# Optimization experiments

Measured on AMD Instinct MI355X. Metric: run time of the kernel, lower is better.

## Reference

```python
import jax, jax.numpy as jnp
import numpy as np

L, V, P, D, H, F = 6, 50257, 1024, 1024, 16, 4096
DH = D // H
EPS = 1e-5


def setup_inputs() -> dict:
    key = jax.random.key(0)
    ks = jax.random.split(key, 8)
    s = 0.02  # init scale to keep activations sane across layers
    inp = {
        "input_ids": jax.random.randint(ks[0], (2, 1024), 0, V),
        "wte": jax.random.normal(ks[1], (V, D), jnp.float32) * s,
        "wpe": jax.random.normal(ks[2], (P, D), jnp.float32) * s,
        "ln1_g": jnp.ones((L, D), jnp.float32),
        "ln1_b": jnp.zeros((L, D), jnp.float32),
        "wq": jax.random.normal(ks[3], (L, D, D), jnp.float32) * s,
        "bq": jnp.zeros((L, D), jnp.float32),
        "wk": jax.random.normal(ks[4], (L, D, D), jnp.float32) * s,
        "bk": jnp.zeros((L, D), jnp.float32),
        "wv": jax.random.normal(ks[5], (L, D, D), jnp.float32) * s,
        "bv": jnp.zeros((L, D), jnp.float32),
        "wo": jax.random.normal(jax.random.fold_in(key, 10), (L, D, D), jnp.float32) * s,
        "bo": jnp.zeros((L, D), jnp.float32),
        "ln2_g": jnp.ones((L, D), jnp.float32),
        "ln2_b": jnp.zeros((L, D), jnp.float32),
        "w1": jax.random.normal(ks[6], (L, D, F), jnp.float32) * s,
        "b1": jnp.zeros((L, F), jnp.float32),
        "w2": jax.random.normal(ks[7], (L, F, D), jnp.float32) * s,
        "b2": jnp.zeros((L, D), jnp.float32),
        "lnf_g": jnp.ones((D,), jnp.float32),
        "lnf_b": jnp.zeros((D,), jnp.float32),
    }
    return inp


def _ln(x, g, b):
    m = jnp.mean(x, axis=-1, keepdims=True)
    v = jnp.mean(jnp.square(x - m), axis=-1, keepdims=True)
    return (x - m) * jax.lax.rsqrt(v + EPS) * g + b


def _block(x, p):
    (g1, be1, wq, bq, wk, bk, wv, bv, wo, bo, g2, be2, w1, b1, w2, b2) = p
    B, T, _ = x.shape
    h = _ln(x, g1, be1)
    q = (h @ wq + bq).reshape(B, T, H, DH)
    k = (h @ wk + bk).reshape(B, T, H, DH)
    v = (h @ wv + bv).reshape(B, T, H, DH)
    scores = jnp.einsum("bqhd,bkhd->bhqk", q, k) * (1.0 / np.sqrt(DH))
    attn = jax.nn.softmax(scores, axis=-1)  # NOTE: no causal mask (as in source)
    o = jnp.einsum("bhqk,bkhd->bqhd", attn, v).reshape(B, T, D)
    x = x + o @ wo + bo
    h2 = _ln(x, g2, be2)
    x = x + jax.nn.gelu(h2 @ w1 + b1, approximate=False) @ w2 + b2
    return x


def reference(input_ids, wte, wpe, ln1_g, ln1_b, wq, bq, wk, bk, wv, bv,
              wo, bo, ln2_g, ln2_b, w1, b1, w2, b2, lnf_g, lnf_b):
    T = input_ids.shape[1]
    x = wte[input_ids] + wpe[:T]  # [B,T,D]
    params = (ln1_g, ln1_b, wq, bq, wk, bk, wv, bv, wo, bo,
              ln2_g, ln2_b, w1, b1, w2, b2)

    def step(x, p):
        return _block(x, p), None

    x, _ = jax.lax.scan(step, x, params)
    return _ln(x, lnf_g, lnf_b)
```

## Files before the change

kernel.cpp:

```cpp
#include <hip/hip_runtime.h>
#include <hip/hip_bf16.h>
#include <math.h>

#define DV 1024
#define FF 4096
#define NLAY 6
#define NH 16
#define TT 1024
#define NTOK 2048

typedef float f32x4 __attribute__((ext_vector_type(4)));
typedef short bf16x8 __attribute__((ext_vector_type(8)));
typedef unsigned short u16;
typedef u16 u16x4 __attribute__((ext_vector_type(4)));
typedef u16 u16x8 __attribute__((ext_vector_type(8)));

__device__ __forceinline__ u16 f2b(float f) {
  unsigned u = __float_as_uint(f);
  unsigned r = (u + 0x7fffu + ((u >> 16) & 1u)) >> 16;
  return (u16)r;
}
__device__ __forceinline__ float b2f(u16 u) {
  return __uint_as_float(((unsigned)u) << 16);
}

__device__ __forceinline__ void gload_lds16(const void* g, void* lds) {
  __builtin_amdgcn_global_load_lds(
      (const __attribute__((address_space(1))) void*)g,
      (__attribute__((address_space(3))) void*)lds, 16, 0, 0);
}

__global__ __launch_bounds__(256) void embed_ln_k(const int* __restrict__ ids,
                                                  const float* __restrict__ wte,
                                                  const float* __restrict__ wpe,
                                                  const float* __restrict__ gg,
                                                  const float* __restrict__ bb,
                                                  float* __restrict__ X,
                                                  u16* __restrict__ outb) {
  int row = blockIdx.x, tid = threadIdx.x;
  int t = row & (TT - 1);
  int id = ids[row];
  f32x4 a = *(const f32x4*)(wte + (size_t)id * DV + tid * 4);
  f32x4 p = *(const f32x4*)(wpe + (size_t)t * DV + tid * 4);
  f32x4 v = a + p;
  *(f32x4*)(X + (size_t)row * DV + tid * 4) = v;
  float s1 = v[0] + v[1] + v[2] + v[3];
  float s2 = v[0] * v[0] + v[1] * v[1] + v[2] * v[2] + v[3] * v[3];
#pragma unroll
  for (int o = 32; o >= 1; o >>= 1) {
    s1 += __shfl_xor(s1, o);
    s2 += __shfl_xor(s2, o);
  }
  __shared__ float sh[8];
  int w = tid >> 6;
  if ((tid & 63) == 0) { sh[w] = s1; sh[w + 4] = s2; }
  __syncthreads();
  s1 = sh[0] + sh[1] + sh[2] + sh[3];
  s2 = sh[4] + sh[5] + sh[6] + sh[7];
  float mean = s1 * (1.0f / DV);
  float var = s2 * (1.0f / DV) - mean * mean;
  float rstd = rsqrtf(var + 1e-5f);
  f32x4 gv = *(const f32x4*)(gg + tid * 4);
  f32x4 bv = *(const f32x4*)(bb + tid * 4);
  u16x4 r;
#pragma unroll
  for (int i = 0; i < 4; ++i) r[i] = f2b((v[i] - mean) * rstd * gv[i] + bv[i]);
  *(u16x4*)(outb + (size_t)row * DV + tid * 4) = r;
}

template <int OUTF>
__global__ __launch_bounds__(256) void ln_k(const float* __restrict__ X,
                                            const float* __restrict__ gg,
                                            const float* __restrict__ bb,
                                            u16* __restrict__ outb,
                                            float* __restrict__ outf) {
  int row = blockIdx.x, tid = threadIdx.x;
  f32x4 v = *(const f32x4*)(X + (size_t)row * DV + tid * 4);
  float s1 = v[0] + v[1] + v[2] + v[3];
  float s2 = v[0] * v[0] + v[1] * v[1] + v[2] * v[2] + v[3] * v[3];
#pragma unroll
  for (int o = 32; o >= 1; o >>= 1) {
    s1 += __shfl_xor(s1, o);
    s2 += __shfl_xor(s2, o);
  }
  __shared__ float sh[8];
  int w = tid >> 6;
  if ((tid & 63) == 0) { sh[w] = s1; sh[w + 4] = s2; }
  __syncthreads();
  s1 = sh[0] + sh[1] + sh[2] + sh[3];
  s2 = sh[4] + sh[5] + sh[6] + sh[7];
  float mean = s1 * (1.0f / DV);
  float var = s2 * (1.0f / DV) - mean * mean;
  float rstd = rsqrtf(var + 1e-5f);
  f32x4 gv = *(const f32x4*)(gg + tid * 4);
  f32x4 bv = *(const f32x4*)(bb + tid * 4);
  f32x4 o;
#pragma unroll
  for (int i = 0; i < 4; ++i) o[i] = (v[i] - mean) * rstd * gv[i] + bv[i];
  if (OUTF) {
    *(f32x4*)(outf + (size_t)row * DV + tid * 4) = o;
  } else {
    u16x4 r = {f2b(o[0]), f2b(o[1]), f2b(o[2]), f2b(o[3])};
    *(u16x4*)(outb + (size_t)row * DV + tid * 4) = r;
  }
}

template <int NS, int OUTF>
__global__ __launch_bounds__(256) void reduce_ln_k(
    float* __restrict__ X, const u16* __restrict__ pp,
    const float* __restrict__ bias, const float* __restrict__ gg,
    const float* __restrict__ bb, u16* __restrict__ outb,
    float* __restrict__ outf) {
  int row = blockIdx.x, tid = threadIdx.x;
  size_t off = (size_t)row * DV + tid * 4;
  f32x4 v = *(const f32x4*)(X + off);
  if (NS > 0) {
    f32x4 bvv = *(const f32x4*)(bias + tid * 4);
    v += bvv;
#pragma unroll
    for (int s = 0; s < NS; ++s) {
      u16x4 pv = *(const u16x4*)(pp + (size_t)s * NTOK * DV + off);
      v[0] += b2f(pv[0]); v[1] += b2f(pv[1]);
      v[2] += b2f(pv[2]); v[3] += b2f(pv[3]);
    }
    *(f32x4*)(X + off) = v;
  }
  float s1 = v[0] + v[1] + v[2] + v[3];
  float s2 = v[0] * v[0] + v[1] * v[1] + v[2] * v[2] + v[3] * v[3];
#pragma unroll
  for (int o = 32; o >= 1; o >>= 1) {
    s1 += __shfl_xor(s1, o);
    s2 += __shfl_xor(s2, o);
  }
  __shared__ float sh[8];
  int w = tid >> 6;
  if ((tid & 63) == 0) { sh[w] = s1; sh[w + 4] = s2; }
  __syncthreads();
  s1 = sh[0] + sh[1] + sh[2] + sh[3];
  s2 = sh[4] + sh[5] + sh[6] + sh[7];
  float mean = s1 * (1.0f / DV);
  float var = s2 * (1.0f / DV) - mean * mean;
  float rstd = rsqrtf(var + 1e-5f);
  f32x4 gv = *(const f32x4*)(gg + tid * 4);
  f32x4 bv = *(const f32x4*)(bb + tid * 4);
  f32x4 o;
#pragma unroll
  for (int i = 0; i < 4; ++i) o[i] = (v[i] - mean) * rstd * gv[i] + bv[i];
  if (OUTF) {
    *(f32x4*)(outf + off) = o;
  } else {
    u16x4 r = {f2b(o[0]), f2b(o[1]), f2b(o[2]), f2b(o[3])};
    *(u16x4*)(outb + off) = r;
  }
}

__global__ __launch_bounds__(256) void transw_k(const float* __restrict__ wq,
                                                const float* __restrict__ wk,
                                                const float* __restrict__ wv,
                                                const float* __restrict__ wo,
                                                const float* __restrict__ w1,
                                                const float* __restrict__ w2,
                                                u16* __restrict__ WT) {
  int lay = blockIdx.y;
  size_t oDD = (size_t)lay * DV * DV, oDF = (size_t)lay * DV * FF;
  u16* WTL = WT + (size_t)lay * 12 * 1024 * 1024;
  int bid = blockIdx.x;
  const float* src;
  u16* dst;
  int K, N, tile;
  if (bid < 256) {
    int which = bid >> 6;
    src = (which == 0 ? wq : which == 1 ? wk : which == 2 ? wv : wo) + oDD;
    dst = WTL + (size_t)which * (DV * DV);
    K = DV; N = DV; tile = bid & 63;
  } else if (bid < 512) {
    src = w1 + oDF; dst = WTL + (size_t)4 * (DV * DV); K = DV; N = FF; tile = bid - 256;
  } else {
    src = w2 + oDF; dst = WTL + (size_t)8 * (DV * DV); K = FF; N = DV; tile = bid - 512;
  }
  int ntc = N >> 8;
  int tr = tile / ntc, tc = tile - tr * ntc;
  int k0 = tr * 64, n0 = tc * 256;
  __shared__ u16 ts[64][258];
  int tid = threadIdx.x, l = tid & 63, w = tid >> 6;
  f32x4 vv[16];
#pragma unroll
  for (int i = 0; i < 16; ++i)
    vv[i] = *(const f32x4*)(src + (size_t)(k0 + i * 4 + w) * N + n0 + l * 4);
#pragma unroll
  for (int i = 0; i < 16; ++i) {
    u16x4 c = {f2b(vv[i][0]), f2b(vv[i][1]), f2b(vv[i][2]), f2b(vv[i][3])};
    *(u16x4*)(&ts[i * 4 + w][l * 4]) = c;
  }
  __syncthreads();
  int kk = (tid & 7) * 8, nn = tid >> 3;
#pragma unroll
  for (int j = 0; j < 8; ++j) {
    int n = j * 32 + nn;
    u16x8 ov;
#pragma unroll
    for (int m = 0; m < 8; ++m) ov[m] = ts[kk + m][n];
    *(u16x8*)(dst + (size_t)(n0 + n) * K + k0 + kk) = ov;
  }
}

template <int EPI>
__global__ __launch_bounds__(256) void gemm_k(
    const u16* __restrict__ A, const u16* __restrict__ Wt,
    const float* __restrict__ b0, const float* __restrict__ b1,
    const float* __restrict__ b2v, u16* __restrict__ o0, u16* __restrict__ o1,
    u16* __restrict__ o2t, u16* __restrict__ op, float* __restrict__ of,
    const float* __restrict__ res, int M, int N, int K, int KS) {
  int z = blockIdx.z;
  const u16* W = Wt;
  const float* bias = b0;
  u16* outb = o0;
  if (EPI == 0) {
    W = Wt + (size_t)z * N * K;
    bias = z == 0 ? b0 : z == 1 ? b1 : b2v;
    outb = z == 0 ? o0 : o1;
  }
  int gx = gridDim.x, nwg = gx * gridDim.y;
  int lin = blockIdx.y * gx + blockIdx.x;
  int cpx = nwg >> 3;
  int swz = (lin & 7) * cpx + (lin >> 3);
  int bm = (swz % gx) * 128, bn = (swz / gx) * 128;
  int kbeg = (EPI == 3) ? z * KS : 0;
  int klen = (EPI == 3) ? KS : K;
  __shared__ __attribute__((aligned(16))) u16 SM[32768];
  u16* As = SM;
  u16* Bs = SM + 16384;
  u16* Cs = SM;
  int tid = threadIdx.x, l = tid & 63, w = tid >> 6;
  int q = l & 15, g = l >> 4;
  int wm = (w >> 1) * 64, wn = (w & 1) * 64;
  int srow = w * 32 + (l >> 3);
  int scol = (((l & 7) ^ ((l >> 3) & 7))) * 8;
  const u16* Ab = A + (size_t)(bm + srow) * K + kbeg + scol;
  const u16* Wb = W + (size_t)(bn + srow) * K + kbeg + scol;
  f32x4 acc[4][4] = {};
  int nk = klen >> 6;
#pragma unroll
  for (int i = 0; i < 4; ++i) {
    gload_lds16(Ab + (size_t)i * 8 * K, &As[(w * 32 + i * 8) * 64]);
    gload_lds16(Wb + (size_t)i * 8 * K, &Bs[(w * 32 + i * 8) * 64]);
  }
  __syncthreads();
  for (int t = 0; t < nk; ++t) {
    int cur = t & 1;
    if (t + 1 < nk) {
      int ko = (t + 1) * 64;
#pragma unroll
      for (int i = 0; i < 4; ++i) {
        gload_lds16(Ab + (size_t)i * 8 * K + ko,
                    &As[(cur ^ 1) * 8192 + (w * 32 + i * 8) * 64]);
        gload_lds16(Wb + (size_t)i * 8 * K + ko,
                    &Bs[(cur ^ 1) * 8192 + (w * 32 + i * 8) * 64]);
      }
    }
#pragma unroll
    for (int kk = 0; kk < 2; ++kk) {
      bf16x8 af[4], bfr[4];
#pragma unroll
      for (int f = 0; f < 4; ++f) {
        int ra = wm + f * 16 + q, rb = wn + f * 16 + q;
        af[f]  = *(const bf16x8*)(&As[cur * 8192 + ra * 64 + ((kk * 4 + g) ^ (ra & 7)) * 8]);
        bfr[f] = *(const bf16x8*)(&Bs[cur * 8192 + rb * 64 + ((kk * 4 + g) ^ (rb & 7)) * 8]);
      }
#pragma unroll
      for (int fm = 0; fm < 4; ++fm)
#pragma unroll
        for (int fn = 0; fn < 4; ++fn)
          acc[fm][fn] = __builtin_amdgcn_mfma_f32_16x16x32_bf16(af[fm], bfr[fn],
                                                                acc[fm][fn], 0, 0, 0);
    }
    __syncthreads();
  }
  if (EPI == 2) {
#pragma unroll
    for (int fm = 0; fm < 4; ++fm)
#pragma unroll
      for (int fn = 0; fn < 4; ++fn) {
        int gcol = bn + wn + fn * 16 + q;
        int growb = bm + wm + fm * 16 + g * 4;
        float bv = bias[gcol];
#pragma unroll
        for (int r = 0; r < 4; ++r)
          of[(size_t)(growb + r) * N + gcol] = res[(size_t)(growb + r) * N + gcol]
                                               + acc[fm][fn][r] + bv;
      }
    return;
  }
  bool tr = (EPI == 0 && z == 2);
#pragma unroll
  for (int fm = 0; fm < 4; ++fm) {
#pragma unroll
    for (int fn = 0; fn < 4; ++fn) {
      int cL = wn + fn * 16 + q;
      float bv = (EPI == 3) ? 0.0f : bias[bn + cL];
#pragma unroll
      for (int r = 0; r < 4; ++r) {
        int rL = wm + fm * 16 + g * 4 + r;
        float v = acc[fm][fn][r] + bv;
        if (EPI == 1) v = 0.5f * v * (1.0f + erff(v * 0.70710678118f));
        if (tr) Cs[cL * 132 + rL] = f2b(v);
        else    Cs[rL * 132 + cL] = f2b(v);
      }
    }
  }
  __syncthreads();
  {
    int rowL = tid >> 4, c8 = (tid & 15) * 8;
#pragma unroll
    for (int p = 0; p < 8; ++p) {
      int row = p * 16 + rowL;
      u16x4 lo = *(const u16x4*)(&Cs[row * 132 + c8]);
      u16x4 hi = *(const u16x4*)(&Cs[row * 132 + c8 + 4]);
      u16x8 ov = {lo[0], lo[1], lo[2], lo[3], hi[0], hi[1], hi[2], hi[3]};
      if (tr) {
        *(u16x8*)(o2t + (size_t)(bn + row) * M + bm + c8) = ov;
      } else if (EPI == 3) {
        *(u16x8*)(op + (size_t)z * M * N + (size_t)(bm + row) * N + bn + c8) = ov;
      } else {
        *(u16x8*)(outb + (size_t)(bm + row) * N + bn + c8) = ov;
      }
    }
  }
}

__global__ __launch_bounds__(256) void attn_k(const u16* __restrict__ Q,
                                              const u16* __restrict__ Kb,
                                              const u16* __restrict__ Vt,
                                              u16* __restrict__ O) {
  int bid = blockIdx.x;
  int qt = bid & 15, h = (bid >> 4) & 15, b = bid >> 8;
  int tid = threadIdx.x, l = tid & 63, w = tid >> 6;
  int q = l & 15, g = l >> 4;
  int tokbase = b * TT;
  int qbase = tokbase + qt * 64 + w * 16;
  __shared__ __attribute__((aligned(16))) u16 Ks[2][32 * 64];
  __shared__ __attribute__((aligned(16))) u16 Vs[2][64 * 32];
  __shared__ __attribute__((aligned(16))) u16 Ps[4][512];
  bf16x8 qf[2];
  {
    int qrow = qbase + q;
#pragma unroll
    for (int half = 0; half < 2; ++half)
      qf[half] = *(const bf16x8*)(Q + (size_t)qrow * DV + h * 64 + half * 32 + g * 8);
  }
  int key_s = w * 8 + (l >> 3), c_s = l & 7;
  const u16* ksrc = Kb + (size_t)(tokbase + key_s) * DV + h * 64 + ((c_s ^ (key_s & 7)) * 8);
  int dl = w * 16 + (l >> 2), c2 = l & 3;
  const u16* vsrc = Vt + (size_t)(h * 64 + dl) * NTOK + tokbase + ((c2 ^ (dl & 3)) * 8);
  f32x4 oacc[4] = {};
  float m_run = -INFINITY, l_run = 0.0f;
  gload_lds16(ksrc, &Ks[0][w * 512]);
  gload_lds16(vsrc, &Vs[0][w * 512]);
  __syncthreads();
  for (int kbk = 0; kbk < TT / 32; ++kbk) {
    int cur = kbk & 1;
    if (kbk + 1 < TT / 32) {
      gload_lds16(ksrc + (size_t)(kbk + 1) * 32 * DV, &Ks[cur ^ 1][w * 512]);
      gload_lds16(vsrc + (kbk + 1) * 32, &Vs[cur ^ 1][w * 512]);
    }
    f32x4 s[2] = {};
#pragma unroll
    for (int kt = 0; kt < 2; ++kt)
#pragma unroll
      for (int half = 0; half < 2; ++half) {
        int row = kt * 16 + q;
        int chunk = (half * 4 + g) ^ (row & 7);
        bf16x8 kf = *(const bf16x8*)(&Ks[cur][row * 64 + chunk * 8]);
        s[kt] = __builtin_amdgcn_mfma_f32_16x16x32_bf16(kf, qf[half], s[kt], 0, 0, 0);
      }
    float tmax = -INFINITY;
#pragma unroll
    for (int kt = 0; kt < 2; ++kt)
#pragma unroll
      for (int r = 0; r < 4; ++r) {
        s[kt][r] *= 0.125f;
        tmax = fmaxf(tmax, s[kt][r]);
      }
    tmax = fmaxf(tmax, __shfl_xor(tmax, 16));
    tmax = fmaxf(tmax, __shfl_xor(tmax, 32));
    float m_new = fmaxf(m_run, tmax);
    float corr = __expf(m_run - m_new);
    float psum = 0.0f;
    u16 pb[2][4];
#pragma unroll
    for (int kt = 0; kt < 2; ++kt)
#pragma unroll
      for (int r = 0; r < 4; ++r) {
        float p = __expf(s[kt][r] - m_new);
        psum += p;
        pb[kt][r] = f2b(p);
      }
    psum += __shfl_xor(psum, 16);
    psum += __shfl_xor(psum, 32);
    l_run = l_run * corr + psum;
    m_run = m_new;
#pragma unroll
    for (int kt = 0; kt < 2; ++kt) {
      u16x4 pv4 = {pb[kt][0], pb[kt][1], pb[kt][2], pb[kt][3]};
      *(u16x4*)(&Ps[w][q * 32 + ((kt * 4 + g) ^ (q & 7)) * 4]) = pv4;
    }
    float corr4[4];
#pragma unroll
    for (int r = 0; r < 4; ++r) corr4[r] = __shfl(corr, g * 4 + r);
#pragma unroll
    for (int nt = 0; nt < 4; ++nt)
#pragma unroll
      for (int r = 0; r < 4; ++r) oacc[nt][r] *= corr4[r];
    u16x4 a0 = *(const u16x4*)(&Ps[w][q * 32 + ((2 * g) ^ (q & 7)) * 4]);
    u16x4 a1 = *(const u16x4*)(&Ps[w][q * 32 + ((2 * g + 1) ^ (q & 7)) * 4]);
    bf16x8 pa = {(short)a0[0], (short)a0[1], (short)a0[2], (short)a0[3],
                 (short)a1[0], (short)a1[1], (short)a1[2], (short)a1[3]};
#pragma unroll
    for (int nt = 0; nt < 4; ++nt) {
      int vrow = nt * 16 + q;
      int vc = g ^ (vrow & 3);
      bf16x8 vf = *(const bf16x8*)(&Vs[cur][vrow * 32 + vc * 8]);
      oacc[nt] = __builtin_amdgcn_mfma_f32_16x16x32_bf16(pa, vf, oacc[nt], 0, 0, 0);
    }
    __syncthreads();
  }
  float rl[4];
#pragma unroll
  for (int r = 0; r < 4; ++r) rl[r] = 1.0f / __shfl(l_run, g * 4 + r);
#pragma unroll
  for (int nt = 0; nt < 4; ++nt)
#pragma unroll
    for (int r = 0; r < 4; ++r) {
      int qrw = qbase + g * 4 + r;
      int d = nt * 16 + q;
      O[(size_t)qrw * DV + h * 64 + d] = f2b(oacc[nt][r] * rl[r]);
    }
}

extern "C" void kernel_launch(void* const* d_in, const int* in_sizes, int n_in,
                              void* d_out, int out_size, void* d_ws, size_t ws_size,
                              hipStream_t stream) {
  const int*   ids = (const int*)d_in[0];
  const float* wte = (const float*)d_in[1];
  const float* wpe = (const float*)d_in[2];
  const float* l1g = (const float*)d_in[3];
  const float* l1b = (const float*)d_in[4];
  const float* wq  = (const float*)d_in[5];
  const float* bq  = (const float*)d_in[6];
  const float* wk  = (const float*)d_in[7];
  const float* bk  = (const float*)d_in[8];
  const float* wv  = (const float*)d_in[9];
  const float* bv  = (const float*)d_in[10];
  const float* wo  = (const float*)d_in[11];
  const float* bo  = (const float*)d_in[12];
  const float* l2g = (const float*)d_in[13];
  const float* l2b = (const float*)d_in[14];
  const float* w1  = (const float*)d_in[15];
  const float* b1  = (const float*)d_in[16];
  const float* w2  = (const float*)d_in[17];
  const float* b2  = (const float*)d_in[18];
  const float* lfg = (const float*)d_in[19];
  const float* lfb = (const float*)d_in[20];
  (void)in_sizes; (void)n_in; (void)out_size;

  bool bigws = ws_size >= ((size_t)221 << 20);
  bool midws = ws_size >= ((size_t)101 << 20);

  char* ws = (char*)d_ws;
  float* x   = (float*)(ws + 0);
  u16*   hb  = (u16*)(ws + ((size_t)8 << 20));
  u16*   qb  = (u16*)(ws + ((size_t)12 << 20));
  u16*   kb  = (u16*)(ws + ((size_t)16 << 20));
  u16*   vbt = (u16*)(ws + ((size_t)20 << 20));
  u16*   ab  = (u16*)(ws + ((size_t)24 << 20));
  u16*   mb  = (u16*)(ws + ((size_t)28 << 20));
  u16*   pp  = (u16*)(ws + ((size_t)44 << 20));
  u16*   WT  = (u16*)(ws + ((size_t)(midws ? 76 : 44) << 20));

  if (bigws)
    transw_k<<<dim3(768, 6), 256, 0, stream>>>(wq, wk, wv, wo, w1, w2, WT);
  embed_ln_k<<<NTOK, 256, 0, stream>>>(ids, wte, wpe, l1g, l1b, x, hb);

  for (int lay = 0; lay < NLAY; ++lay) {
    size_t oDD = (size_t)lay * DV * DV;
    size_t oDF = (size_t)lay * DV * FF;
    u16* WTL = bigws ? WT + (size_t)lay * 12 * 1024 * 1024 : WT;
    if (!bigws)
      transw_k<<<dim3(768, 1), 256, 0, stream>>>(wq + oDD, wk + oDD, wv + oDD,
                                                 wo + oDD, w1 + oDF, w2 + oDF, WTL);
    gemm_k<0><<<dim3(16, 8, 3), 256, 0, stream>>>(
        hb, WTL, bq + lay * DV, bk + lay * DV, bv + lay * DV,
        qb, kb, vbt, nullptr, nullptr, nullptr, NTOK, DV, DV, 0);
    attn_k<<<512, 256, 0, stream>>>(qb, kb, vbt, ab);
    if (midws) {
      gemm_k<3><<<dim3(16, 8, 2), 256, 0, stream>>>(
          ab, WTL + (size_t)3 * DV * DV, nullptr, nullptr, nullptr,
          nullptr, nullptr, nullptr, pp, nullptr, nullptr, NTOK, DV, DV, 512);
      reduce_ln_k<2, 0><<<NTOK, 256, 0, stream>>>(
          x, pp, bo + lay * DV, l2g + lay * DV, l2b + lay * DV, hb, nullptr);
    } else {
      gemm_k<2><<<dim3(16, 8, 1), 256, 0, stream>>>(
          ab, WTL + (size_t)3 * DV * DV, bo + lay * DV, nullptr, nullptr,
          nullptr, nullptr, nullptr, nullptr, x, x, NTOK, DV, DV, 0);
      ln_k<0><<<NTOK, 256, 0, stream>>>(x, l2g + lay * DV, l2b + lay * DV, hb, nullptr);
    }
    gemm_k<1><<<dim3(16, 32, 1), 256, 0, stream>>>(
        hb, WTL + (size_t)4 * DV * DV, b1 + lay * FF, nullptr, nullptr,
        mb, nullptr, nullptr, nullptr, nullptr, nullptr, NTOK, FF, DV, 0);
    if (midws) {
      gemm_k<3><<<dim3(16, 8, 4), 256, 0, stream>>>(
          mb, WTL + (size_t)8 * DV * DV, nullptr, nullptr, nullptr,
          nullptr, nullptr, nullptr, pp, nullptr, nullptr, NTOK, DV, FF, 1024);
      if (lay < NLAY - 1)
        reduce_ln_k<4, 0><<<NTOK, 256, 0, stream>>>(
            x, pp, b2 + lay * DV, l1g + (lay + 1) * DV, l1b + (lay + 1) * DV,
            hb, nullptr);
      else
        reduce_ln_k<4, 1><<<NTOK, 256, 0, stream>>>(
            x, pp, b2 + lay * DV, lfg, lfb, nullptr, (float*)d_out);
    } else {
      gemm_k<2><<<dim3(16, 8, 1), 256, 0, stream>>>(
          mb, WTL + (size_t)8 * DV * DV, b2 + lay * DV, nullptr, nullptr,
          nullptr, nullptr, nullptr, nullptr, x, x, NTOK, DV, FF, 0);
      if (lay < NLAY - 1)
        ln_k<0><<<NTOK, 256, 0, stream>>>(x, l1g + (lay + 1) * DV,
                                          l1b + (lay + 1) * DV, hb, nullptr);
      else
        ln_k<1><<<NTOK, 256, 0, stream>>>(x, lfg, lfb, nullptr, (float*)d_out);
    }
  }
}
```

Measured before the change: 946.0 us.

## Widen attention key tiles to 64, fold Q scale into projection, lazy rescale

```diff
diff --git a/kernel.cpp b/kernel.cpp
--- a/kernel.cpp
+++ b/kernel.cpp
@@ -303,6 +303,7 @@
         int rL = wm + fm * 16 + g * 4 + r;
         float v = acc[fm][fn][r] + bv;
         if (EPI == 1) v = 0.5f * v * (1.0f + erff(v * 0.70710678118f));
+        if (EPI == 0 && z == 0) v *= 0.125f;
         if (tr) Cs[cL * 132 + rL] = f2b(v);
         else    Cs[rL * 132 + cL] = f2b(v);
       }
@@ -338,9 +339,9 @@
   int q = l & 15, g = l >> 4;
   int tokbase = b * TT;
   int qbase = tokbase + qt * 64 + w * 16;
-  __shared__ __attribute__((aligned(16))) u16 Ks[2][32 * 64];
-  __shared__ __attribute__((aligned(16))) u16 Vs[2][64 * 32];
-  __shared__ __attribute__((aligned(16))) u16 Ps[4][512];
+  __shared__ __attribute__((aligned(16))) u16 Ks[2][64 * 64];
+  __shared__ __attribute__((aligned(16))) u16 Vs[2][64 * 64];
+  __shared__ __attribute__((aligned(16))) u16 Ps[4][1024];
   bf16x8 qf[2];
   {
     int qrow = qbase + q;
@@ -348,82 +349,91 @@
     for (int half = 0; half < 2; ++half)
       qf[half] = *(const bf16x8*)(Q + (size_t)qrow * DV + h * 64 + half * 32 + g * 8);
   }
-  int key_s = w * 8 + (l >> 3), c_s = l & 7;
-  const u16* ksrc = Kb + (size_t)(tokbase + key_s) * DV + h * 64 + ((c_s ^ (key_s & 7)) * 8);
-  int dl = w * 16 + (l >> 2), c2 = l & 3;
-  const u16* vsrc = Vt + (size_t)(h * 64 + dl) * NTOK + tokbase + ((c2 ^ (dl & 3)) * 8);
+  int rr = tid >> 3, cc = tid & 7;
+  const u16* ksrc = Kb + (size_t)(tokbase + rr) * DV + h * 64 + ((cc ^ (rr & 7)) * 8);
+  const u16* vsrc = Vt + (size_t)(h * 64 + rr) * NTOK + tokbase + ((cc ^ (rr & 7)) * 8);
+  const size_t kst = (size_t)32 * DV;
+  const size_t vst = (size_t)32 * NTOK;
   f32x4 oacc[4] = {};
   float m_run = -INFINITY, l_run = 0.0f;
-  gload_lds16(ksrc, &Ks[0][w * 512]);
-  gload_lds16(vsrc, &Vs[0][w * 512]);
-  __syncthreads();
-  for (int kbk = 0; kbk < TT / 32; ++kbk) {
+#define AST(bb_, t)                                                      \
+  {                                                                      \
+    gload_lds16(ksrc + (size_t)(t) * 64 * DV, &Ks[bb_][tid * 8]);        \
+    gload_lds16(ksrc + (size_t)(t) * 64 * DV + kst, &Ks[bb_][2048 + tid * 8]); \
+    gload_lds16(vsrc + (t) * 64, &Vs[bb_][tid * 8]);                     \
+    gload_lds16(vsrc + (t) * 64 + vst, &Vs[bb_][2048 + tid * 8]);        \
+  }
+  AST(0, 0);
+  __syncthreads();
+  const int nkb = TT / 64;
+  for (int kbk = 0; kbk < nkb; ++kbk) {
     int cur = kbk & 1;
-    if (kbk + 1 < TT / 32) {
-      gload_lds16(ksrc + (size_t)(kbk + 1) * 32 * DV, &Ks[cur ^ 1][w * 512]);
-      gload_lds16(vsrc + (kbk + 1) * 32, &Vs[cur ^ 1][w * 512]);
-    }
-    f32x4 s[2] = {};
-#pragma unroll
-    for (int kt = 0; kt < 2; ++kt)
+    if (kbk + 1 < nkb) AST(cur ^ 1, kbk + 1);
+    f32x4 s[4] = {};
+#pragma unroll
+    for (int kt = 0; kt < 4; ++kt) {
+      int row = kt * 16 + q;
 #pragma unroll
       for (int half = 0; half < 2; ++half) {
-        int row = kt * 16 + q;
         int chunk = (half * 4 + g) ^ (row & 7);
         bf16x8 kf = *(const bf16x8*)(&Ks[cur][row * 64 + chunk * 8]);
         s[kt] = __builtin_amdgcn_mfma_f32_16x16x32_bf16(kf, qf[half], s[kt], 0, 0, 0);
       }
+    }
     float tmax = -INFINITY;
 #pragma unroll
-    for (int kt = 0; kt < 2; ++kt)
-#pragma unroll
-      for (int r = 0; r < 4; ++r) {
-        s[kt][r] *= 0.125f;
-        tmax = fmaxf(tmax, s[kt][r]);
-      }
+    for (int kt = 0; kt < 4; ++kt)
+#pragma unroll
+      for (int r = 0; r < 4; ++r) tmax = fmaxf(tmax, s[kt][r]);
     tmax = fmaxf(tmax, __shfl_xor(tmax, 16));
     tmax = fmaxf(tmax, __shfl_xor(tmax, 32));
-    float m_new = fmaxf(m_run, tmax);
-    float corr = __expf(m_run - m_new);
+    if (!__all(tmax <= m_run + 8.0f)) {
+      float m_new = fmaxf(m_run, tmax);
+      float corr = __expf(m_run - m_new);
+      float corr4[4];
+#pragma unroll
+      for (int r = 0; r < 4; ++r) corr4[r] = __shfl(corr, g * 4 + r);
+#pragma unroll
+      for (int nt = 0; nt < 4; ++nt)
+#pragma unroll
+        for (int r = 0; r < 4; ++r) oacc[nt][r] *= corr4[r];
+      l_run *= corr;
+      m_run = m_new;
+    }
     float psum = 0.0f;
-    u16 pb[2][4];
-#pragma unroll
-    for (int kt = 0; kt < 2; ++kt)
+    u16x4 pb[4];
+#pragma unroll
+    for (int kt = 0; kt < 4; ++kt)
 #pragma unroll
       for (int r = 0; r < 4; ++r) {
-        float p = __expf(s[kt][r] - m_new);
+        float p = __expf(s[kt][r] - m_run);
         psum += p;
         pb[kt][r] = f2b(p);
       }
     psum += __shfl_xor(psum, 16);
     psum += __shfl_xor(psum, 32);
-    l_run = l_run * corr + psum;
-    m_run = m_new;
-#pragma unroll
-    for (int kt = 0; kt < 2; ++kt) {
-      u16x4 pv4 = {pb[kt][0], pb[kt][1], pb[kt][2], pb[kt][3]};
-      *(u16x4*)(&Ps[w][q * 32 + ((kt * 4 + g) ^ (q & 7)) * 4]) = pv4;
-    }
-    float corr4[4];
-#pragma unroll
-    for (int r = 0; r < 4; ++r) corr4[r] = __shfl(corr, g * 4 + r);
-#pragma unroll
-    for (int nt = 0; nt < 4; ++nt)
-#pragma unroll
-      for (int r = 0; r < 4; ++r) oacc[nt][r] *= corr4[r];
-    u16x4 a0 = *(const u16x4*)(&Ps[w][q * 32 + ((2 * g) ^ (q & 7)) * 4]);
-    u16x4 a1 = *(const u16x4*)(&Ps[w][q * 32 + ((2 * g + 1) ^ (q & 7)) * 4]);
-    bf16x8 pa = {(short)a0[0], (short)a0[1], (short)a0[2], (short)a0[3],
-                 (short)a1[0], (short)a1[1], (short)a1[2], (short)a1[3]};
-#pragma unroll
-    for (int nt = 0; nt < 4; ++nt) {
-      int vrow = nt * 16 + q;
-      int vc = g ^ (vrow & 3);
-      bf16x8 vf = *(const bf16x8*)(&Vs[cur][vrow * 32 + vc * 8]);
-      oacc[nt] = __builtin_amdgcn_mfma_f32_16x16x32_bf16(pa, vf, oacc[nt], 0, 0, 0);
+    l_run += psum;
+#pragma unroll
+    for (int kt = 0; kt < 4; ++kt)
+      *(u16x4*)(&Ps[w][q * 64 + ((kt * 4 + g) ^ (q & 7)) * 4]) = pb[kt];
+#pragma unroll
+    for (int kt2 = 0; kt2 < 2; ++kt2) {
+      int c0 = kt2 * 8 + (g >> 1) * 4 + (g & 1) * 2;
+      u16x4 a0 = *(const u16x4*)(&Ps[w][q * 64 + ((c0) ^ (q & 7)) * 4]);
+      u16x4 a1 = *(const u16x4*)(&Ps[w][q * 64 + ((c0 + 1) ^ (q & 7)) * 4]);
+      bf16x8 pa = {(short)a0[0], (short)a0[1], (short)a0[2], (short)a0[3],
+                   (short)a1[0], (short)a1[1], (short)a1[2], (short)a1[3]};
+#pragma unroll
+      for (int nt = 0; nt < 4; ++nt) {
+        int vrow = nt * 16 + q;
+        int vc = (kt2 * 4 + g) ^ (vrow & 7);
+        bf16x8 vf = *(const bf16x8*)(&Vs[cur][vrow * 64 + vc * 8]);
+        oacc[nt] = __builtin_amdgcn_mfma_f32_16x16x32_bf16(pa, vf, oacc[nt], 0, 0, 0);
+      }
     }
     __syncthreads();
   }
+#undef AST
   float rl[4];
 #pragma unroll
   for (int r = 0; r < 4; ++r) rl[r] = 1.0f / __shfl(l_run, g * 4 + r);
```

Result: faster. 888.1 us (-6.1%).
